# Kernel optimization log

Measured on AMD Instinct MI355X. Metric: run time of the kernel, lower is better.

The kernel has to match this reference:

```python
import jax, jax.numpy as jnp
import numpy as np

K = 3       # kernel size
STRIDE = 1
PAD = 1
BN_EPS = 1e-5


def setup_inputs() -> dict:
    key = jax.random.key(0)
    ks = jax.random.split(key, 5)
    B, C, H, W = 4, 64, 128, 128
    OC = 64
    x = jax.random.normal(ks[0], (B, C, H, W), dtype=jnp.float32)
    # offset conv weights scaled small so predicted offsets are a few pixels
    w_off = jax.random.normal(ks[1], (2 * K * K, C, K, K), dtype=jnp.float32) * 0.01
    b_off = jnp.zeros((2 * K * K,), dtype=jnp.float32)
    fan_in = C * K * K
    w_def = jax.random.normal(ks[2], (OC, C, K, K), dtype=jnp.float32) / np.sqrt(fan_in)
    b_def = jnp.zeros((OC,), dtype=jnp.float32)
    gamma = jnp.ones((OC,), dtype=jnp.float32)
    beta = jnp.zeros((OC,), dtype=jnp.float32)
    prelu_w = jnp.full((OC,), 0.2, dtype=jnp.float32)  # nn.PReLU(init=0.2)
    return {"x": x, "w_off": w_off, "b_off": b_off, "w_def": w_def,
            "b_def": b_def, "gamma": gamma, "beta": beta, "prelu_w": prelu_w}


def _conv2d(x, w, b):
    out = jax.lax.conv_general_dilated(
        x, w, window_strides=(STRIDE, STRIDE),
        padding=[(PAD, PAD), (PAD, PAD)],
        dimension_numbers=("NCHW", "OIHW", "NCHW"))
    return out + b[None, :, None, None]


def _deform_conv(x, offset, w, b):
    """torchvision-style deform_conv2d (groups=1, no modulation)."""
    B, C, H, W = x.shape
    OC = w.shape[0]
    Ho, Wo = offset.shape[2], offset.shape[3]
    kk = K * K
    off = offset.reshape(B, kk, 2, Ho, Wo)
    dy, dx = off[:, :, 0], off[:, :, 1]                 # [B,kk,Ho,Wo]
    kh = (jnp.arange(kk) // K).astype(jnp.float32)
    kw = (jnp.arange(kk) % K).astype(jnp.float32)
    ys = (jnp.arange(Ho) * STRIDE - PAD).astype(jnp.float32)
    xs = (jnp.arange(Wo) * STRIDE - PAD).astype(jnp.float32)
    py = ys[None, None, :, None] + kh[None, :, None, None] + dy   # [B,kk,Ho,Wo]
    px = xs[None, None, None, :] + kw[None, :, None, None] + dx

    y0 = jnp.floor(py); x0 = jnp.floor(px)
    wy1 = py - y0; wy0 = 1.0 - wy1
    wx1 = px - x0; wx0 = 1.0 - wx1
    x_flat = x.reshape(B, C, H * W)

    def corner(yf, xf, wgt):
        yi = yf.astype(jnp.int32); xi = xf.astype(jnp.int32)
        valid = (yi >= 0) & (yi < H) & (xi >= 0) & (xi < W)
        yi = jnp.clip(yi, 0, H - 1); xi = jnp.clip(xi, 0, W - 1)
        idx = (yi * W + xi).reshape(B, 1, -1)           # [B,1,kk*Ho*Wo]
        vals = jnp.take_along_axis(x_flat, idx, axis=2)  # [B,C,kk*Ho*Wo]
        wm = (wgt * valid.astype(wgt.dtype)).reshape(B, 1, -1)
        return vals * wm

    samp = (corner(y0, x0, wy0 * wx0) + corner(y0, x0 + 1, wy0 * wx1)
            + corner(y0 + 1, x0, wy1 * wx0) + corner(y0 + 1, x0 + 1, wy1 * wx1))
    samp = samp.reshape(B, C, kk, Ho, Wo)
    out = jnp.einsum("bckhw,ock->bohw", samp, w.reshape(OC, C, kk))
    return out + b[None, :, None, None]


def reference(x, w_off, b_off, w_def, b_def, gamma, beta, prelu_w):
    offset = _conv2d(x, w_off, b_off)
    y = _deform_conv(x, offset, w_def, b_def)
    # BatchNorm2d (training-mode batch stats)
    mean = jnp.mean(y, axis=(0, 2, 3), keepdims=True)
    var = jnp.var(y, axis=(0, 2, 3), keepdims=True)
    y = (y - mean) * jax.lax.rsqrt(var + BN_EPS)
    y = y * gamma[None, :, None, None] + beta[None, :, None, None]
    # PReLU per-channel
    return jnp.where(y >= 0, y, prelu_w[None, :, None, None] * y)
```

## Files before the change

kernel.cpp:

```cpp
#include <hip/hip_runtime.h>

#define BSZ 4
#define CIN 64
#define HH 128
#define WW 128
#define OCH 64
#define HWSZ (HH*WW)
#define KK 9
#define NPIX (BSZ*HH*WW)

typedef __attribute__((ext_vector_type(8))) short short8v;
typedef __attribute__((ext_vector_type(8))) unsigned short ushort8v;
typedef __attribute__((ext_vector_type(4))) float float4v;

#define Y_OFF     0
#define WTB_OFF   2097152
#define WOFB_OFF  (WTB_OFF + 18432)
#define STATS_OFF (WOFB_OFF + 9216)

__device__ __forceinline__ short f2bf(float f) {
    unsigned u = __builtin_bit_cast(unsigned, f);
    unsigned r = (u + 0x7FFFu + ((u >> 16) & 1u)) >> 16;
    return (short)r;
}
__device__ __forceinline__ float bf2f(unsigned short u) {
    return __builtin_bit_cast(float, ((unsigned)u) << 16);
}

__global__ void prep_w(const float* __restrict__ w_def,
                       const float* __restrict__ w_off,
                       short* __restrict__ wtb,
                       short* __restrict__ wofb) {
    int i = blockIdx.x * 256 + threadIdx.x;
    if (i < 36864) {
        int oc = i / 576, rr = i % 576;
        int c = rr / 9, k = rr % 9;
        wtb[(k * OCH + oc) * CIN + c] = f2bf(w_def[i]);
    } else if (i < 36864 + 18432) {
        int j = i - 36864;
        int o = j / 576, rr = j % 576;
        int tap = rr / 64, c = rr % 64;
        wofb[j] = (o < 18) ? f2bf(w_off[(o * 64 + c) * 9 + tap]) : (short)0;
    }
}

__global__ __launch_bounds__(256, 8) void transpose_x(const float* __restrict__ x,
                                                      unsigned short* __restrict__ xt) {
    __shared__ float t[64][33];
    const int bid = blockIdx.x;
    const int wg  = (bid & 7) * 256 + (bid >> 3);
    const int tid = threadIdx.x;
    const int gp0 = wg * 32;
    const int b   = gp0 >> 14;
    const int hw0 = gp0 & 16383;
    const float* src = x + b * CIN * HWSZ + hw0;
    #pragma unroll
    for (int pass = 0; pass < 8; ++pass) {
        int c = pass * 8 + (tid >> 5);
        int p = tid & 31;
        t[c][p] = src[c * HWSZ + p];
    }
    __syncthreads();
    unsigned short* dst = xt + (b * HWSZ + hw0) * 64;
    #pragma unroll
    for (int pass = 0; pass < 8; ++pass) {
        int p = pass * 4 + (tid >> 6);
        int c = tid & 63;
        dst[p * 64 + c] = (unsigned short)f2bf(t[c][p]);
    }
}

__global__ __launch_bounds__(256, 4) void deform_fused(
    const unsigned short* __restrict__ xt,
    const short* __restrict__ wofb,
    const float* __restrict__ b_off,
    const short* __restrict__ wtb,
    const float* __restrict__ b_def,
    unsigned short* __restrict__ ybuf,
    float* __restrict__ gsum,
    float* __restrict__ gsq)
{
    __shared__ float off_lds[18][64];
    __shared__ float red0[4][64];
    __shared__ float red1[4][64];

    const int bid  = blockIdx.x;
    const int r    = (bid & 7) * 128 + (bid >> 3);
    const int tid  = threadIdx.x;
    const int lane = tid & 63;
    const int wv   = tid >> 6;
    const int b    = r >> 8;
    const int rem  = r & 255;
    const int ho   = rem >> 1, half = rem & 1;
    const int l15  = lane & 15;
    const int l4   = lane >> 4;
    const int cbase = l4 * 8;
    const int p    = half * 64 + wv * 16 + l15;

    const unsigned short* xb = xt + b * HWSZ * 64;

    {
        float4v offacc0 = (float4v){0.f, 0.f, 0.f, 0.f};
        float4v offacc1 = (float4v){0.f, 0.f, 0.f, 0.f};
        const ushort8v zero8 = {0, 0, 0, 0, 0, 0, 0, 0};
        #pragma unroll
        for (int kk = 0; kk < 18; ++kk) {
            const int tap = kk >> 1;
            const int kh = tap / 3, kw = tap % 3;
            const int yy = ho - 1 + kh;
            const int xx = p - 1 + kw;
            const bool valid = ((unsigned)yy < (unsigned)HH) & ((unsigned)xx < (unsigned)WW);
            const int pix = valid ? (yy * WW + xx) : 0;
            ushort8v bo = *(const ushort8v*)(xb + pix * 64 + (kk & 1) * 32 + cbase);
            if (!valid) bo = zero8;
            short8v bos = __builtin_bit_cast(short8v, bo);
            short8v af0 = *(const short8v*)(wofb + (l15) * 576 + kk * 32 + cbase);
            short8v af1 = *(const short8v*)(wofb + (16 + l15) * 576 + kk * 32 + cbase);
            offacc0 = __builtin_amdgcn_mfma_f32_16x16x32_bf16(af0, bos, offacc0, 0, 0, 0);
            offacc1 = __builtin_amdgcn_mfma_f32_16x16x32_bf16(af1, bos, offacc1, 0, 0, 0);
        }
        const int col = wv * 16 + l15;
        #pragma unroll
        for (int rr = 0; rr < 4; ++rr) {
            int row = l4 * 4 + rr;
            off_lds[row][col] = offacc0[rr] + b_off[row];
        }
        if (l4 == 0) {
            #pragma unroll
            for (int rr = 0; rr < 2; ++rr) {
                int row = 16 + rr;
                off_lds[row][col] = offacc1[rr] + b_off[row];
            }
        }
    }
    __syncthreads();

    float och[18];
    {
        const int col = wv * 16 + l15;
        #pragma unroll
        for (int j = 0; j < 18; ++j) och[j] = off_lds[j][col];
    }

    float4v acc[4];
    #pragma unroll
    for (int mt = 0; mt < 4; ++mt) acc[mt] = (float4v){0.f, 0.f, 0.f, 0.f};

    #pragma unroll
    for (int k = 0; k < KK; ++k) {
        float dy = och[2 * k];
        float dx = och[2 * k + 1];
        float py = (float)(ho - 1 + (k / 3)) + dy;
        float px = (float)(p - 1 + (k % 3)) + dx;
        float y0f = floorf(py), x0f = floorf(px);
        int y0 = (int)y0f, x0 = (int)x0f;
        float wy1 = py - y0f, wy0 = 1.f - wy1;
        float wx1 = px - x0f, wx0 = 1.f - wx1;
        int vy0 = ((unsigned)y0 < (unsigned)HH), vy1 = ((unsigned)(y0 + 1) < (unsigned)HH);
        int vx0 = ((unsigned)x0 < (unsigned)WW), vx1 = ((unsigned)(x0 + 1) < (unsigned)WW);
        float w00 = wy0 * wx0 * (float)(vy0 & vx0);
        float w01 = wy0 * wx1 * (float)(vy0 & vx1);
        float w10 = wy1 * wx0 * (float)(vy1 & vx0);
        float w11 = wy1 * wx1 * (float)(vy1 & vx1);
        int y0c = min(max(y0, 0), HH - 1), y1c = min(max(y0 + 1, 0), HH - 1);
        int x0c = min(max(x0, 0), WW - 1), x1c = min(max(x0 + 1, 0), WW - 1);
        const unsigned short* p00 = xb + (y0c * WW + x0c) * 64 + cbase;
        const unsigned short* p01 = xb + (y0c * WW + x1c) * 64 + cbase;
        const unsigned short* p10 = xb + (y1c * WW + x0c) * 64 + cbase;
        const unsigned short* p11 = xb + (y1c * WW + x1c) * 64 + cbase;

        ushort8v g00a = *(const ushort8v*)(p00);
        ushort8v g01a = *(const ushort8v*)(p01);
        ushort8v g10a = *(const ushort8v*)(p10);
        ushort8v g11a = *(const ushort8v*)(p11);
        ushort8v g00b = *(const ushort8v*)(p00 + 32);
        ushort8v g01b = *(const ushort8v*)(p01 + 32);
        ushort8v g10b = *(const ushort8v*)(p10 + 32);
        ushort8v g11b = *(const ushort8v*)(p11 + 32);

        short8v Bf[2];
        #pragma unroll
        for (int j = 0; j < 8; ++j) {
            float v = bf2f(g00a[j]) * w00 + bf2f(g01a[j]) * w01
                    + bf2f(g10a[j]) * w10 + bf2f(g11a[j]) * w11;
            Bf[0][j] = f2bf(v);
        }
        #pragma unroll
        for (int j = 0; j < 8; ++j) {
            float v = bf2f(g00b[j]) * w00 + bf2f(g01b[j]) * w01
                    + bf2f(g10b[j]) * w10 + bf2f(g11b[j]) * w11;
            Bf[1][j] = f2bf(v);
        }

        const short* wk = wtb + k * OCH * CIN;
        #pragma unroll
        for (int mt = 0; mt < 4; ++mt) {
            const short* wrow = wk + (mt * 16 + l15) * CIN + cbase;
            #pragma unroll
            for (int kc = 0; kc < 2; ++kc) {
                short8v Af = *(const short8v*)(wrow + kc * 32);
                acc[mt] = __builtin_amdgcn_mfma_f32_16x16x32_bf16(Af, Bf[kc], acc[mt], 0, 0, 0);
            }
        }
    }

    float lsum[4][4], lsq[4][4];
    const int yrow = ho * WW;
    #pragma unroll
    for (int mt = 0; mt < 4; ++mt) {
        #pragma unroll
        for (int rr = 0; rr < 4; ++rr) {
            const int oc = mt * 16 + l4 * 4 + rr;
            float v = acc[mt][rr] + b_def[oc];
            ybuf[(b * OCH + oc) * HWSZ + yrow + p] = (unsigned short)f2bf(v);
            lsum[mt][rr] = v;
            lsq[mt][rr]  = v * v;
        }
    }
    #pragma unroll
    for (int m = 1; m <= 8; m <<= 1) {
        #pragma unroll
        for (int mt = 0; mt < 4; ++mt)
            #pragma unroll
            for (int rr = 0; rr < 4; ++rr) {
                lsum[mt][rr] += __shfl_xor(lsum[mt][rr], m);
                lsq[mt][rr]  += __shfl_xor(lsq[mt][rr], m);
            }
    }
    if (l15 == 0) {
        #pragma unroll
        for (int mt = 0; mt < 4; ++mt)
            #pragma unroll
            for (int rr = 0; rr < 4; ++rr) {
                const int oc = mt * 16 + l4 * 4 + rr;
                red0[wv][oc] = lsum[mt][rr];
                red1[wv][oc] = lsq[mt][rr];
            }
    }
    __syncthreads();
    if (tid < 128) {
        const int oc = tid & 63, s = tid >> 6;
        if (s == 0) {
            float v = red0[0][oc] + red0[1][oc] + red0[2][oc] + red0[3][oc];
            atomicAdd(&gsum[oc], v);
        } else {
            float v = red1[0][oc] + red1[1][oc] + red1[2][oc] + red1[3][oc];
            atomicAdd(&gsq[oc], v);
        }
    }
}

__global__ void finalize_bn(const float* __restrict__ gsum, const float* __restrict__ gsq,
                            const float* __restrict__ gamma, const float* __restrict__ beta,
                            float* __restrict__ ss) {
    int c = threadIdx.x;
    if (c < OCH) {
        const float inv = 1.f / (float)NPIX;
        float mean = gsum[c] * inv;
        float var = gsq[c] * inv - mean * mean;
        float rstd = rsqrtf(var + 1e-5f);
        float sc = gamma[c] * rstd;
        ss[c] = sc;
        ss[OCH + c] = beta[c] - mean * sc;
    }
}

__global__ __launch_bounds__(256) void apply_bn(const unsigned short* __restrict__ ybuf,
                                                const float* __restrict__ ss,
                                                const float* __restrict__ prelu,
                                                float* __restrict__ out) {
    int i = blockIdx.x * 256 + threadIdx.x;
    int oc = ((i * 8) >> 14) & 63;
    float sc = ss[oc], sh = ss[OCH + oc], pw = prelu[oc];
    ushort8v v8 = ((const ushort8v*)ybuf)[i];
    float4 o0, o1;
    float t;
    t = fmaf(bf2f(v8[0]), sc, sh); o0.x = t >= 0.f ? t : pw * t;
    t = fmaf(bf2f(v8[1]), sc, sh); o0.y = t >= 0.f ? t : pw * t;
    t = fmaf(bf2f(v8[2]), sc, sh); o0.z = t >= 0.f ? t : pw * t;
    t = fmaf(bf2f(v8[3]), sc, sh); o0.w = t >= 0.f ? t : pw * t;
    t = fmaf(bf2f(v8[4]), sc, sh); o1.x = t >= 0.f ? t : pw * t;
    t = fmaf(bf2f(v8[5]), sc, sh); o1.y = t >= 0.f ? t : pw * t;
    t = fmaf(bf2f(v8[6]), sc, sh); o1.z = t >= 0.f ? t : pw * t;
    t = fmaf(bf2f(v8[7]), sc, sh); o1.w = t >= 0.f ? t : pw * t;
    ((float4*)out)[i * 2]     = o0;
    ((float4*)out)[i * 2 + 1] = o1;
}

extern "C" void kernel_launch(void* const* d_in, const int* in_sizes, int n_in,
                              void* d_out, int out_size, void* d_ws, size_t ws_size,
                              hipStream_t stream) {
    const float* x      = (const float*)d_in[0];
    const float* w_off  = (const float*)d_in[1];
    const float* b_off  = (const float*)d_in[2];
    const float* w_def  = (const float*)d_in[3];
    const float* b_def  = (const float*)d_in[4];
    const float* gamma  = (const float*)d_in[5];
    const float* beta   = (const float*)d_in[6];
    const float* prelu  = (const float*)d_in[7];

    float* ws    = (float*)d_ws;
    unsigned short* ybuf = (unsigned short*)(ws + Y_OFF);
    short* wtb   = (short*)(ws + WTB_OFF);
    short* wofb  = (short*)(ws + WOFB_OFF);
    float* stats = ws + STATS_OFF;
    float* gsum  = stats;
    float* gsq   = stats + OCH;
    float* ss    = stats + 2 * OCH;

    unsigned short* xt = (unsigned short*)d_out;

    hipMemsetAsync(stats, 0, 2 * OCH * sizeof(float), stream);
    prep_w<<<216, 256, 0, stream>>>(w_def, w_off, wtb, wofb);
    transpose_x<<<BSZ * HWSZ / 32, 256, 0, stream>>>(x, xt);
    deform_fused<<<BSZ * HH * 2, 256, 0, stream>>>(xt, wofb, b_off, wtb, b_def, ybuf, gsum, gsq);
    finalize_bn<<<1, 64, 0, stream>>>(gsum, gsq, gamma, beta, ss);
    apply_bn<<<(BSZ * OCH * HWSZ) / 8 / 256, 256, 0, stream>>>(ybuf, ss, prelu, (float*)d_out);
}
```

Measured before the change: 190.8 us.

## Stage 6-row input band in LDS for offset conv and bilinear gathers

Each block now loads a swizzled 6-row by 80-column bf16 band of the channel-last input into shared memory. Both the offset convolution taps and the bilinear sampling corners read from this band, with a fallback to global memory when a sample falls outside it. The goal is to replace scattered global gathers with LDS reads, and the XOR swizzle is there to avoid bank conflicts. The band takes about 61KB of LDS, so the launch bound is lowered to 2 blocks per CU, which may reduce latency hiding. The stats zeroing memset is also folded into prep_w to save one launch.

```diff
diff --git a/kernel.cpp b/kernel.cpp
--- a/kernel.cpp
+++ b/kernel.cpp
@@ -30,8 +30,10 @@
 __global__ void prep_w(const float* __restrict__ w_def,
                        const float* __restrict__ w_off,
                        short* __restrict__ wtb,
-                       short* __restrict__ wofb) {
+                       short* __restrict__ wofb,
+                       float* __restrict__ stats) {
     int i = blockIdx.x * 256 + threadIdx.x;
+    if (blockIdx.x == 0 && threadIdx.x < 128) stats[threadIdx.x] = 0.f;
     if (i < 36864) {
         int oc = i / 576, rr = i % 576;
         int c = rr / 9, k = rr % 9;
@@ -70,7 +72,7 @@
     }
 }
 
-__global__ __launch_bounds__(256, 4) void deform_fused(
+__global__ __launch_bounds__(256, 2) void deform_fused(
     const unsigned short* __restrict__ xt,
     const short* __restrict__ wofb,
     const float* __restrict__ b_off,
@@ -80,6 +82,7 @@
     float* __restrict__ gsum,
     float* __restrict__ gsq)
 {
+    __shared__ unsigned short band[6 * 80 * 64];
     __shared__ float off_lds[18][64];
     __shared__ float red0[4][64];
     __shared__ float red1[4][64];
@@ -96,8 +99,24 @@
     const int l4   = lane >> 4;
     const int cbase = l4 * 8;
     const int p    = half * 64 + wv * 16 + l15;
+    const int wx0  = half * 64 - 8;
 
     const unsigned short* xb = xt + b * HWSZ * 64;
+    char* bandc = (char*)band;
+
+    #pragma unroll
+    for (int i = 0; i < 15; ++i) {
+        int G  = i * 256 + tid;
+        int g  = G & 7;
+        int xs = (G >> 3) % 80;
+        int rs = G / 640;
+        int row = min(max(ho - 2 + rs, 0), HH - 1);
+        int col = min(max(wx0 + xs, 0), WW - 1);
+        ushort8v v = *(const ushort8v*)(xb + (row * WW + col) * 64 + g * 8);
+        int dstB = ((rs * 80 + xs) << 7) + ((g ^ (xs & 7)) << 4);
+        *(ushort8v*)(bandc + dstB) = v;
+    }
+    __syncthreads();
 
     {
         float4v offacc0 = (float4v){0.f, 0.f, 0.f, 0.f};
@@ -110,9 +129,13 @@
             const int yy = ho - 1 + kh;
             const int xx = p - 1 + kw;
             const bool valid = ((unsigned)yy < (unsigned)HH) & ((unsigned)xx < (unsigned)WW);
-            const int pix = valid ? (yy * WW + xx) : 0;
-            ushort8v bo = *(const ushort8v*)(xb + pix * 64 + (kk & 1) * 32 + cbase);
-            if (!valid) bo = zero8;
+            ushort8v bo = zero8;
+            if (valid) {
+                int xs = xx - wx0;
+                int q  = l4 + (kk & 1) * 4;
+                int adr = (((kh + 1) * 80 + xs) << 7) + ((q ^ (xs & 7)) << 4);
+                bo = *(const ushort8v*)(bandc + adr);
+            }
             short8v bos = __builtin_bit_cast(short8v, bo);
             short8v af0 = *(const short8v*)(wofb + (l15) * 576 + kk * 32 + cbase);
             short8v af1 = *(const short8v*)(wofb + (16 + l15) * 576 + kk * 32 + cbase);
@@ -155,28 +178,46 @@
         float y0f = floorf(py), x0f = floorf(px);
         int y0 = (int)y0f, x0 = (int)x0f;
         float wy1 = py - y0f, wy0 = 1.f - wy1;
-        float wx1 = px - x0f, wx0 = 1.f - wx1;
+        float wx1 = px - x0f, wx0f_ = 1.f - wx1;
         int vy0 = ((unsigned)y0 < (unsigned)HH), vy1 = ((unsigned)(y0 + 1) < (unsigned)HH);
         int vx0 = ((unsigned)x0 < (unsigned)WW), vx1 = ((unsigned)(x0 + 1) < (unsigned)WW);
-        float w00 = wy0 * wx0 * (float)(vy0 & vx0);
-        float w01 = wy0 * wx1 * (float)(vy0 & vx1);
-        float w10 = wy1 * wx0 * (float)(vy1 & vx0);
-        float w11 = wy1 * wx1 * (float)(vy1 & vx1);
+        float w00 = wy0 * wx0f_ * (float)(vy0 & vx0);
+        float w01 = wy0 * wx1  * (float)(vy0 & vx1);
+        float w10 = wy1 * wx0f_ * (float)(vy1 & vx0);
+        float w11 = wy1 * wx1  * (float)(vy1 & vx1);
         int y0c = min(max(y0, 0), HH - 1), y1c = min(max(y0 + 1, 0), HH - 1);
         int x0c = min(max(x0, 0), WW - 1), x1c = min(max(x0 + 1, 0), WW - 1);
-        const unsigned short* p00 = xb + (y0c * WW + x0c) * 64 + cbase;
-        const unsigned short* p01 = xb + (y0c * WW + x1c) * 64 + cbase;
-        const unsigned short* p10 = xb + (y1c * WW + x0c) * 64 + cbase;
-        const unsigned short* p11 = xb + (y1c * WW + x1c) * 64 + cbase;
-
-        ushort8v g00a = *(const ushort8v*)(p00);
-        ushort8v g01a = *(const ushort8v*)(p01);
-        ushort8v g10a = *(const ushort8v*)(p10);
-        ushort8v g11a = *(const ushort8v*)(p11);
-        ushort8v g00b = *(const ushort8v*)(p00 + 32);
-        ushort8v g01b = *(const ushort8v*)(p01 + 32);
-        ushort8v g10b = *(const ushort8v*)(p10 + 32);
-        ushort8v g11b = *(const ushort8v*)(p11 + 32);
+
+        int sy0 = y0c - (ho - 2), sy1 = y1c - (ho - 2);
+        int sx0 = x0c - wx0,      sx1 = x1c - wx0;
+        bool inb = (sy0 >= 0) & (sy1 < 6) & (sx0 >= 0) & (sx1 < 80);
+
+        ushort8v g00a, g01a, g10a, g11a, g00b, g01b, g10b, g11b;
+        if (__builtin_expect(inb, 1)) {
+            const int qa = l4, qb = l4 + 4;
+            int a00 = ((sy0 * 80 + sx0) << 7);
+            int a01 = ((sy0 * 80 + sx1) << 7);
+            int a10 = ((sy1 * 80 + sx0) << 7);
+            int a11 = ((sy1 * 80 + sx1) << 7);
+            int h0 = (sx0 & 7), h1 = (sx1 & 7);
+            g00a = *(const ushort8v*)(bandc + a00 + ((qa ^ h0) << 4));
+            g01a = *(const ushort8v*)(bandc + a01 + ((qa ^ h1) << 4));
+            g10a = *(const ushort8v*)(bandc + a10 + ((qa ^ h0) << 4));
+            g11a = *(const ushort8v*)(bandc + a11 + ((qa ^ h1) << 4));
+            g00b = *(const ushort8v*)(bandc + a00 + ((qb ^ h0) << 4));
+            g01b = *(const ushort8v*)(bandc + a01 + ((qb ^ h1) << 4));
+            g10b = *(const ushort8v*)(bandc + a10 + ((qb ^ h0) << 4));
+            g11b = *(const ushort8v*)(bandc + a11 + ((qb ^ h1) << 4));
+        } else {
+            const unsigned short* p00 = xb + (y0c * WW + x0c) * 64 + cbase;
+            const unsigned short* p01 = xb + (y0c * WW + x1c) * 64 + cbase;
+            const unsigned short* p10 = xb + (y1c * WW + x0c) * 64 + cbase;
+            const unsigned short* p11 = xb + (y1c * WW + x1c) * 64 + cbase;
+            g00a = *(const ushort8v*)(p00);      g01a = *(const ushort8v*)(p01);
+            g10a = *(const ushort8v*)(p10);      g11a = *(const ushort8v*)(p11);
+            g00b = *(const ushort8v*)(p00 + 32); g01b = *(const ushort8v*)(p01 + 32);
+            g10b = *(const ushort8v*)(p10 + 32); g11b = *(const ushort8v*)(p11 + 32);
+        }
 
         short8v Bf[2];
         #pragma unroll
@@ -310,8 +351,7 @@
 
     unsigned short* xt = (unsigned short*)d_out;
 
-    hipMemsetAsync(stats, 0, 2 * OCH * sizeof(float), stream);
-    prep_w<<<216, 256, 0, stream>>>(w_def, w_off, wtb, wofb);
+    prep_w<<<216, 256, 0, stream>>>(w_def, w_off, wtb, wofb, stats);
     transpose_x<<<BSZ * HWSZ / 32, 256, 0, stream>>>(x, xt);
     deform_fused<<<BSZ * HH * 2, 256, 0, stream>>>(xt, wofb, b_off, wtb, b_def, ybuf, gsum, gsq);
     finalize_bn<<<1, 64, 0, stream>>>(gsum, gsq, gamma, beta, ss);
```

New measurement: 173.9 us. 8.9% less time.
